# Kernel optimization log

Measured on AMD Instinct MI355X. Metric: run time of the kernel, lower is better.

Reference implementation:

```python
import jax, jax.numpy as jnp
import numpy as np

B, D, N, PT_DEPTH = 1024, 1024, 128, 28
TOPK_FRAC = 0.25
NOISE_EPS = 0.01

def setup_inputs() -> dict:
    key = jax.random.key(0)
    ks = jax.random.split(key, 10)
    s = 0.02
    return {
        "prompt_embeddings": jax.random.normal(ks[0], (PT_DEPTH, N, D), jnp.float32) * s,
        "w1": jax.random.normal(ks[1], (D, 1), jnp.float32) * s,      # Linear(1, D) weight [out,in]
        "b1": jnp.zeros((D,), jnp.float32),
        "w2": jax.random.normal(ks[2], (D, D), jnp.float32) * s,      # Linear(D, D)
        "b2": jnp.zeros((D,), jnp.float32),
        "gate_w": jax.random.normal(ks[3], (N, D + 1), jnp.float32) * s,  # Linear(D+1, N)
        "gate_b": jnp.zeros((N,), jnp.float32),
        "w_noise": jax.random.normal(ks[4], (D, N), jnp.float32) * s,
        "noise": jax.random.normal(ks[5], (B, N), jnp.float32),
        "timestep": jax.random.randint(ks[6], (B,), 0, PT_DEPTH, jnp.int64),
    }

def reference(prompt_embeddings, w1, b1, w2, b2, gate_w, gate_b, w_noise, noise, timestep):
    step = timestep[0]  # scalar index, like timestep[0].item()
    t = timestep.astype(jnp.float32)[:, None]                    # [B, 1]
    # timestep embedder: Linear -> SiLU -> Linear
    t_embed = jax.nn.silu(t @ w1.T + b1) @ w2.T + b2             # [B, D]
    prompts = prompt_embeddings[step]                            # [N, D]
    # noisy top-k gating
    depth_col = jnp.full((t_embed.shape[0], 1), 0.0, jnp.float32) + step.astype(jnp.float32)
    gate_in = jnp.concatenate([t_embed, depth_col], axis=-1)     # [B, D+1]
    clean_logits = gate_in @ gate_w.T + gate_b                   # [B, N]
    noise_std = jax.nn.softplus(t_embed @ w_noise) + NOISE_EPS   # [B, N]
    noisy_logits = clean_logits + noise * noise_std
    k = min(int(TOPK_FRAC * N) + 1, N)                           # 33 (static)
    top_logits, top_idx = jax.lax.top_k(noisy_logits, k)
    top_k_gates = jax.nn.softmax(top_logits[:, : k - 1], axis=-1)  # [B, k-1]
    rows = jnp.arange(noisy_logits.shape[0])[:, None]
    gates = jnp.zeros_like(noisy_logits).at[rows, top_idx[:, : k - 1]].set(top_k_gates)  # [B, N]
    out = prompts[None, :, :] * gates[:, :, None]                # [B, N, D]
    return out, t_embed
```

## Files before the change

kernel.cpp:

```cpp
#include <hip/hip_runtime.h>
#include <math.h>

#define B_ 1024
#define D_ 1024
#define N_ 128
#define PT_ 28
#define KSEL 32
#define NOISE_EPS_ 0.01f

typedef float fx4 __attribute__((ext_vector_type(4)));

__global__ __launch_bounds__(256) void embed_kernel(
    const float* __restrict__ w1, const float* __restrict__ b1,
    const float* __restrict__ w2, const float* __restrict__ b2,
    float* __restrict__ ue)
{
    __shared__ __align__(16) float h[D_];
    const int s = blockIdx.x;
    const int tid = threadIdx.x;
    const float sf = (float)s;
    for (int d = tid; d < D_; d += 256) {
        float x = sf * w1[d] + b1[d];
        h[d] = x / (1.0f + expf(-x));
    }
    __syncthreads();
    const int wave = tid >> 6;
    const int lane = tid & 63;
    const fx4* __restrict__ h4 = (const fx4*)h;
    for (int j = 0; j < 32; ++j) {
        const int i = blockIdx.y * 128 + wave * 32 + j;
        const fx4* __restrict__ row = (const fx4*)(w2 + (size_t)i * D_);
        float acc = 0.0f;
        #pragma unroll
        for (int k = 0; k < 4; ++k) {
            fx4 u  = row[k * 64 + lane];
            fx4 hv = h4 [k * 64 + lane];
            acc += u.x * hv.x + u.y * hv.y + u.z * hv.z + u.w * hv.w;
        }
        #pragma unroll
        for (int off = 32; off; off >>= 1) acc += __shfl_down(acc, off, 64);
        if (lane == 0) ue[(size_t)s * D_ + i] = acc + b2[i];
    }
}

__global__ __launch_bounds__(256) void gate_precompute_kernel(
    const float* __restrict__ gate_w, const float* __restrict__ gate_b,
    const float* __restrict__ w_noise, const int* __restrict__ timestep,
    const float* __restrict__ ue, float* __restrict__ uclean, float* __restrict__ unstd)
{
    __shared__ __align__(16) float te[D_];
    __shared__ float pcl[N_];
    __shared__ float pnz[2][N_];
    const int s = blockIdx.x;
    const int tid = threadIdx.x;
    for (int d = tid; d < D_; d += 256) te[d] = ue[(size_t)s * D_ + d];
    __syncthreads();
    const int wave = tid >> 6;
    const int lane = tid & 63;

    for (int j = 0; j < 32; ++j) {
        const int n = wave * 32 + j;
        const float* __restrict__ grow = gate_w + (size_t)n * (D_ + 1);
        float acc = 0.0f;
        #pragma unroll
        for (int k = 0; k < 16; ++k)
            acc += grow[k * 64 + lane] * te[k * 64 + lane];
        #pragma unroll
        for (int off = 32; off; off >>= 1) acc += __shfl_down(acc, off, 64);
        if (lane == 0) pcl[n] = acc;
    }

    {
        const int n = (wave & 1) * 64 + lane;
        const int dbase = (wave >> 1) * 512;
        float acc = 0.0f;
        for (int d = 0; d < 512; ++d)
            acc += te[dbase + d] * w_noise[(size_t)(dbase + d) * N_ + n];
        pnz[wave >> 1][n] = acc;
    }
    __syncthreads();

    if (tid < N_) {
        const int step = timestep[0];
        float cl2 = pcl[tid]
                  + (float)step * gate_w[(size_t)tid * (D_ + 1) + D_]
                  + gate_b[tid];
        uclean[s * N_ + tid] = cl2;
        float nz2 = pnz[0][tid] + pnz[1][tid];
        float sp = (nz2 > 20.0f) ? nz2 : log1pf(expf(nz2));
        unstd[s * N_ + tid] = sp + NOISE_EPS_;
    }
}

__global__ __launch_bounds__(256) void out_kernel(
    const float* __restrict__ pe,
    const float* __restrict__ noise,
    const int* __restrict__ timestep,
    const float* __restrict__ ue, const float* __restrict__ uclean,
    const float* __restrict__ unstd,
    float* __restrict__ out0, float* __restrict__ out1)
{
    __shared__ float noisy[N_];
    __shared__ float gates[N_];
    __shared__ float inv_sum;
    const int b = blockIdx.x;
    const int tid = threadIdx.x;
    const int tb = timestep[b];
    const int step = timestep[0];

    if (tid < N_) {
        noisy[tid] = uclean[tb * N_ + tid]
                   + noise[(size_t)b * N_ + tid] * unstd[tb * N_ + tid];
    }

    {
        const fx4* __restrict__ uer = (const fx4*)(ue + (size_t)tb * D_);
        fx4* __restrict__ o1 = (fx4*)(out1 + (size_t)b * D_);
        for (int i = tid; i < D_ / 4; i += 256)
            __builtin_nontemporal_store(uer[i], o1 + i);
    }
    __syncthreads();

    if (tid < N_) {
        const float v = noisy[tid];
        int rank = 0; float mx = -INFINITY;
        for (int m = 0; m < N_; ++m) {
            float u = noisy[m];
            mx = fmaxf(mx, u);
            rank += ((u > v) || (u == v && m < tid)) ? 1 : 0;
        }
        gates[tid] = (rank < KSEL) ? expf(v - mx) : 0.0f;
    }
    __syncthreads();
    if (tid < 64) {
        float s2 = gates[tid] + gates[tid + 64];
        #pragma unroll
        for (int off = 32; off; off >>= 1) s2 += __shfl_down(s2, off, 64);
        if (tid == 0) inv_sum = 1.0f / s2;
    }
    __syncthreads();
    if (tid < N_) gates[tid] *= inv_sum;
    __syncthreads();

    const fx4* __restrict__ psrc = (const fx4*)(pe + (size_t)step * N_ * D_);
    fx4* __restrict__ pdst = (fx4*)(out0 + (size_t)b * N_ * D_);
    for (int it = 0; it < N_; ++it) {
        const float g = gates[it];
        const int idx = it * 256 + tid;
        fx4 o;
        if (g != 0.0f) {
            fx4 u = psrc[idx];
            o = u * g;
        } else {
            o = (fx4)0.0f;
        }
        __builtin_nontemporal_store(o, pdst + idx);
    }
}

extern "C" void kernel_launch(void* const* d_in, const int* in_sizes, int n_in,
                              void* d_out, int out_size, void* d_ws, size_t ws_size,
                              hipStream_t stream) {
    (void)in_sizes; (void)n_in; (void)out_size; (void)ws_size;
    const float* pe      = (const float*)d_in[0];
    const float* w1      = (const float*)d_in[1];
    const float* b1      = (const float*)d_in[2];
    const float* w2      = (const float*)d_in[3];
    const float* b2      = (const float*)d_in[4];
    const float* gate_w  = (const float*)d_in[5];
    const float* gate_b  = (const float*)d_in[6];
    const float* w_noise = (const float*)d_in[7];
    const float* noise   = (const float*)d_in[8];
    const int*   ts      = (const int*)d_in[9];

    float* ws     = (float*)d_ws;
    float* ue     = ws;
    float* uclean = ue + PT_ * D_;
    float* unstd  = uclean + PT_ * N_;

    float* out0 = (float*)d_out;
    float* out1 = out0 + (size_t)B_ * N_ * D_;

    hipLaunchKernelGGL(embed_kernel, dim3(PT_, 8), dim3(256), 0, stream,
                       w1, b1, w2, b2, ue);
    hipLaunchKernelGGL(gate_precompute_kernel, dim3(PT_), dim3(256), 0, stream,
                       gate_w, gate_b, w_noise, ts, ue, uclean, unstd);
    hipLaunchKernelGGL(out_kernel, dim3(B_), dim3(256), 0, stream,
                       pe, noise, ts, ue, uclean, unstd, out0, out1);
}
```

Measured before the change: 628.9 us.

## Split gating into separate kernel and quarter the output broadcast across blocks

Moves the per-row noisy top-k gate computation and the t_embed copy into a dedicated 128-thread kernel that writes normalized gates to workspace. The large output kernel now runs on a 1024x4 grid, each block covering 32 prompts, so it starts streaming stores immediately without the serial rank loop in front. The aim is more parallelism and less per-block latency in the bandwidth-bound 512MB write. The cost is an extra launch and a small gates round trip through global memory.

```diff
diff --git a/kernel.cpp b/kernel.cpp
--- a/kernel.cpp
+++ b/kernel.cpp
@@ -92,68 +92,66 @@
     }
 }
 
-__global__ __launch_bounds__(256) void out_kernel(
-    const float* __restrict__ pe,
-    const float* __restrict__ noise,
-    const int* __restrict__ timestep,
+__global__ __launch_bounds__(128) void gates_kernel(
+    const float* __restrict__ noise, const int* __restrict__ timestep,
     const float* __restrict__ ue, const float* __restrict__ uclean,
     const float* __restrict__ unstd,
-    float* __restrict__ out0, float* __restrict__ out1)
+    float* __restrict__ gates_g, float* __restrict__ out1)
 {
     __shared__ float noisy[N_];
-    __shared__ float gates[N_];
-    __shared__ float inv_sum;
+    __shared__ float wsum[2];
     const int b = blockIdx.x;
     const int tid = threadIdx.x;
     const int tb = timestep[b];
+    const float v = uclean[tb * N_ + tid]
+                  + noise[(size_t)b * N_ + tid] * unstd[tb * N_ + tid];
+    noisy[tid] = v;
+    __syncthreads();
+    int rank = 0; float mx = -INFINITY;
+    for (int m = 0; m < N_; ++m) {
+        float u = noisy[m];
+        mx = fmaxf(mx, u);
+        rank += ((u > v) || (u == v && m < tid)) ? 1 : 0;
+    }
+    float g = (rank < KSEL) ? expf(v - mx) : 0.0f;
+    float s2 = g;
+    #pragma unroll
+    for (int off = 32; off; off >>= 1) s2 += __shfl_down(s2, off, 64);
+    if ((tid & 63) == 0) wsum[tid >> 6] = s2;
+    __syncthreads();
+    const float inv = 1.0f / (wsum[0] + wsum[1]);
+    gates_g[(size_t)b * N_ + tid] = g * inv;
+
+    const fx4* __restrict__ uer = (const fx4*)(ue + (size_t)tb * D_);
+    fx4* __restrict__ o1 = (fx4*)(out1 + (size_t)b * D_);
+    #pragma unroll
+    for (int i = 0; i < 2; ++i)
+        __builtin_nontemporal_store(uer[i * 128 + tid], o1 + i * 128 + tid);
+}
+
+__global__ __launch_bounds__(256) void out_kernel(
+    const float* __restrict__ pe,
+    const int* __restrict__ timestep,
+    const float* __restrict__ gates_g,
+    float* __restrict__ out0)
+{
+    __shared__ float sg[32];
+    const int b = blockIdx.x, q = blockIdx.y;
+    const int tid = threadIdx.x;
     const int step = timestep[0];
-
-    if (tid < N_) {
-        noisy[tid] = uclean[tb * N_ + tid]
-                   + noise[(size_t)b * N_ + tid] * unstd[tb * N_ + tid];
-    }
-
-    {
-        const fx4* __restrict__ uer = (const fx4*)(ue + (size_t)tb * D_);
-        fx4* __restrict__ o1 = (fx4*)(out1 + (size_t)b * D_);
-        for (int i = tid; i < D_ / 4; i += 256)
-            __builtin_nontemporal_store(uer[i], o1 + i);
-    }
+    if (tid < 32) sg[tid] = gates_g[(size_t)b * N_ + q * 32 + tid];
     __syncthreads();
-
-    if (tid < N_) {
-        const float v = noisy[tid];
-        int rank = 0; float mx = -INFINITY;
-        for (int m = 0; m < N_; ++m) {
-            float u = noisy[m];
-            mx = fmaxf(mx, u);
-            rank += ((u > v) || (u == v && m < tid)) ? 1 : 0;
-        }
-        gates[tid] = (rank < KSEL) ? expf(v - mx) : 0.0f;
-    }
-    __syncthreads();
-    if (tid < 64) {
-        float s2 = gates[tid] + gates[tid + 64];
-        #pragma unroll
-        for (int off = 32; off; off >>= 1) s2 += __shfl_down(s2, off, 64);
-        if (tid == 0) inv_sum = 1.0f / s2;
-    }
-    __syncthreads();
-    if (tid < N_) gates[tid] *= inv_sum;
-    __syncthreads();
-
-    const fx4* __restrict__ psrc = (const fx4*)(pe + (size_t)step * N_ * D_);
-    fx4* __restrict__ pdst = (fx4*)(out0 + (size_t)b * N_ * D_);
-    for (int it = 0; it < N_; ++it) {
-        const float g = gates[it];
-        const int idx = it * 256 + tid;
+    const fx4* __restrict__ psrc =
+        (const fx4*)(pe + (size_t)step * N_ * D_) + (size_t)q * 32 * (D_ / 4);
+    fx4* __restrict__ pdst =
+        (fx4*)(out0 + (size_t)b * N_ * D_) + (size_t)q * 32 * (D_ / 4);
+    #pragma unroll 4
+    for (int it = 0; it < 32; ++it) {
+        const float g = sg[it];
+        const int idx = it * (D_ / 4) + tid;
         fx4 o;
-        if (g != 0.0f) {
-            fx4 u = psrc[idx];
-            o = u * g;
-        } else {
-            o = (fx4)0.0f;
-        }
+        if (g != 0.0f) o = psrc[idx] * g;
+        else           o = (fx4)0.0f;
         __builtin_nontemporal_store(o, pdst + idx);
     }
 }
@@ -173,10 +171,11 @@
     const float* noise   = (const float*)d_in[8];
     const int*   ts      = (const int*)d_in[9];
 
-    float* ws     = (float*)d_ws;
-    float* ue     = ws;
-    float* uclean = ue + PT_ * D_;
-    float* unstd  = uclean + PT_ * N_;
+    float* ws      = (float*)d_ws;
+    float* ue      = ws;
+    float* uclean  = ue + PT_ * D_;
+    float* unstd   = uclean + PT_ * N_;
+    float* gates_g = unstd + PT_ * N_;
 
     float* out0 = (float*)d_out;
     float* out1 = out0 + (size_t)B_ * N_ * D_;
@@ -185,6 +184,8 @@
                        w1, b1, w2, b2, ue);
     hipLaunchKernelGGL(gate_precompute_kernel, dim3(PT_), dim3(256), 0, stream,
                        gate_w, gate_b, w_noise, ts, ue, uclean, unstd);
-    hipLaunchKernelGGL(out_kernel, dim3(B_), dim3(256), 0, stream,
-                       pe, noise, ts, ue, uclean, unstd, out0, out1);
+    hipLaunchKernelGGL(gates_kernel, dim3(B_), dim3(128), 0, stream,
+                       noise, ts, ue, uclean, unstd, gates_g, out1);
+    hipLaunchKernelGGL(out_kernel, dim3(B_, 4), dim3(256), 0, stream,
+                       pe, ts, gates_g, out0);
 }
```

Result: no change. 630.5 us (+0.2%).
